# Optimization experiments

Hardware: AMD Instinct MI355X
Metric: run time of the kernel (lower is better)

The kernel has to match this reference:

```python
import jax, jax.numpy as jnp
import numpy as np

N_NODES = 50000
N_EDGES = 1600000
F_IN = 512      # 2 * embedding_dimension
HID = 512
OUT = 4
NEG_SLOPE = 0.01  # torch LeakyReLU default


def _leaky_relu(x):
    return jnp.where(x >= 0, x, NEG_SLOPE * x)


def setup_inputs() -> dict:
    key = jax.random.key(0)
    ks = jax.random.split(key, 12)
    s_in = 1.0 / np.sqrt(F_IN)
    s_h = 1.0 / np.sqrt(HID)
    return {
        "feature": jax.random.normal(ks[0], (N_NODES, F_IN), jnp.float32),
        "edge_index": jax.random.randint(ks[1], (2, N_EDGES), 0, N_NODES, jnp.int64),
        "edge_type": jax.random.randint(ks[2], (N_EDGES,), 0, 2, jnp.int64),
        # input MLP
        "W_in": jax.random.uniform(ks[3], (F_IN, HID), jnp.float32, -s_in, s_in),
        "b_in": jnp.zeros((HID,), jnp.float32),
        # sage1: lin_l (bias) on aggregated neighbors, lin_r (no bias) on self
        "W1_l": jax.random.uniform(ks[4], (HID, HID), jnp.float32, -s_h, s_h),
        "b1_l": jnp.zeros((HID,), jnp.float32),
        "W1_r": jax.random.uniform(ks[5], (HID, HID), jnp.float32, -s_h, s_h),
        # sage2
        "W2_l": jax.random.uniform(ks[6], (HID, HID), jnp.float32, -s_h, s_h),
        "b2_l": jnp.zeros((HID,), jnp.float32),
        "W2_r": jax.random.uniform(ks[7], (HID, HID), jnp.float32, -s_h, s_h),
        # output linear (hidden -> 4); note forward skips linear_relu_output1
        "W_out": jax.random.uniform(ks[8], (HID, OUT), jnp.float32, -s_h, s_h),
        "b_out": jnp.zeros((OUT,), jnp.float32),
    }


def _sage_conv(x, src, dst, W_l, b_l, W_r):
    # mean aggregation of source features onto destinations (PyG default flow)
    agg = jax.ops.segment_sum(x[src], dst, num_segments=N_NODES)  # [N, H]
    cnt = jax.ops.segment_sum(jnp.ones((src.shape[0], 1), x.dtype), dst,
                              num_segments=N_NODES)               # [N, 1]
    mean = agg / jnp.maximum(cnt, 1.0)
    return mean @ W_l + b_l + x @ W_r


def reference(feature, edge_index, edge_type,
              W_in, b_in, W1_l, b1_l, W1_r, W2_l, b2_l, W2_r, W_out, b_out):
    src, dst = edge_index[0], edge_index[1]
    x = _leaky_relu(feature.astype(jnp.float32) @ W_in + b_in)
    x = _sage_conv(x, src, dst, W1_l, b1_l, W1_r)
    # dropout is identity in eval mode
    x = _sage_conv(x, src, dst, W2_l, b2_l, W2_r)
    return x @ W_out + b_out
```

## Files before the change

### kernel.cpp

```cpp
#include <hip/hip_runtime.h>
#include <stdint.h>

#define NNODES 50000
#define NEDGES 1600000
#define HID 512
#define NEG_SLOPE 0.01f
#define NBUCK 98
#define NBLK 200
#define TILE 8000
#define NSUB 8
#define GPBLK 391
#define MROWS 50048

#define ZTOT4 263040
#define ZBLK 1028
#define TCBLK 1024
#define CABLK 12512
#define SABLK 1025
#define PREP_TC (ZBLK)
#define PREP_CA (ZBLK + TCBLK)
#define PREP_SA (ZBLK + TCBLK + CABLK)
#define PREP_FLAG (ZBLK + TCBLK + CABLK + SABLK)
#define PREP_GRID (PREP_FLAG + 1)

typedef __attribute__((ext_vector_type(8))) short bf16x8;
typedef __attribute__((ext_vector_type(8))) unsigned short u16x8;
typedef __attribute__((ext_vector_type(4))) float f32x4;

__device__ __forceinline__ unsigned short f2bf(float f) {
  unsigned int u = __builtin_bit_cast(unsigned int, f);
  u += 0x7FFFu + ((u >> 16) & 1u);
  return (unsigned short)(u >> 16);
}
__device__ __forceinline__ void gload_lds16(const void* g, void* l) {
  __builtin_amdgcn_global_load_lds(
      (const __attribute__((address_space(1))) void*)g,
      (__attribute__((address_space(3))) void*)l, 16, 0, 0);
}

__device__ __forceinline__ float wave_dot(const float* __restrict__ Arow,
                                          const float* __restrict__ B, int j) {
  int l = threadIdx.x & 63;
  float4 a0 = *reinterpret_cast<const float4*>(Arow + l * 8);
  float4 a1 = *reinterpret_cast<const float4*>(Arow + l * 8 + 4);
  const float* bb = B + (size_t)(l * 8) * 4 + j;
  float s = a0.x * bb[0] + a0.y * bb[4] + a0.z * bb[8] + a0.w * bb[12] +
            a1.x * bb[16] + a1.y * bb[20] + a1.z * bb[24] + a1.w * bb[28];
#pragma unroll
  for (int off = 1; off < 64; off <<= 1) s += __shfl_xor(s, off);
  return s;
}

__global__ __launch_bounds__(256) void prep(
    const float* __restrict__ feat, const float* __restrict__ W_in,
    const float* __restrict__ W2l, const float* __restrict__ W2r,
    const float* __restrict__ Wout, const float* __restrict__ b2l,
    const float* __restrict__ bout, const int* __restrict__ ei,
    float* __restrict__ zbase, unsigned short* __restrict__ Wt0,
    unsigned short* __restrict__ featb,
    float* __restrict__ Wlp, float* __restrict__ Wrp, float* __restrict__ bp,
    int* __restrict__ flag) {
  int blk = blockIdx.x, t = threadIdx.x;
  if (blk < PREP_TC) {
    int idx = blk * 256 + t;
    if (idx < ZTOT4) reinterpret_cast<float4*>(zbase)[idx] = {0.f, 0.f, 0.f, 0.f};
  } else if (blk < PREP_CA) {
    int i = (blk - PREP_TC) * 256 + t;
    int n = i >> 9, k = i & 511;
    Wt0[i] = f2bf(W_in[(k << 9) | n]);
  } else if (blk < PREP_SA) {
    int idx = (blk - PREP_CA) * 256 + t;
    size_t g = (size_t)idx * 8;
    int row = idx >> 6;
    u16x8 pk;
    if (row < NNODES) {
      float4 v0 = *reinterpret_cast<const float4*>(feat + g);
      float4 v1 = *reinterpret_cast<const float4*>(feat + g + 4);
      pk[0] = f2bf(v0.x); pk[1] = f2bf(v0.y); pk[2] = f2bf(v0.z); pk[3] = f2bf(v0.w);
      pk[4] = f2bf(v1.x); pk[5] = f2bf(v1.y); pk[6] = f2bf(v1.z); pk[7] = f2bf(v1.w);
    } else {
      pk = (u16x8)0;
    }
    *reinterpret_cast<u16x8*>(featb + g) = pk;
  } else if (blk < PREP_FLAG) {
    int gw = (blk - PREP_SA) * 4 + (t >> 6);
    int l = t & 63;
    if (gw < 2048) {
      float v = wave_dot(W2l + (size_t)(gw >> 2) * 512, Wout, gw & 3);
      if (l == 0) Wlp[gw] = v;
    } else if (gw < 4096) {
      int g = gw - 2048;
      float v = wave_dot(W2r + (size_t)(g >> 2) * 512, Wout, g & 3);
      if (l == 0) Wrp[g] = v;
    } else if (gw < 4100) {
      int j = gw - 4096;
      float v = wave_dot(b2l, Wout, j);
      if (l == 0) bp[j] = v + bout[j];
    }
  } else {
    if (t < 64) {
      unsigned long long m = __ballot(ei[2 * t + 1] != 0);
      if (t == 0) *flag = (m != 0ULL) ? 1 : 0;
    }
  }
}

__global__ __launch_bounds__(256) void smallB(
    const float* __restrict__ W1l, const float* __restrict__ W1r,
    const float* __restrict__ b1l,
    const float* __restrict__ Wlp, const float* __restrict__ Wrp,
    const float* __restrict__ bp,
    float* __restrict__ Pall, float* __restrict__ kb, float* __restrict__ kc) {
  int gw = blockIdx.x * 4 + (threadIdx.x >> 6);
  int l = threadIdx.x & 63;
  if (gw < 6144) {
    int k = gw / 12, jg = gw % 12;
    int g = jg >> 2, j = jg & 3;
    float v;
    if (g == 0) v = wave_dot(W1l + (size_t)k * 512, Wlp, j);
    else if (g == 1) v = wave_dot(W1r + (size_t)k * 512, Wlp, j) +
                         wave_dot(W1l + (size_t)k * 512, Wrp, j);
    else v = wave_dot(W1r + (size_t)k * 512, Wrp, j);
    if (l == 0) Pall[k * 12 + jg] = v;
  } else if (gw < 6152) {
    int i = gw - 6144, j = i & 3;
    if (i < 4) {
      float v = wave_dot(b1l, Wlp, j);
      if (l == 0) kb[j] = v;
    } else {
      float v = wave_dot(b1l, Wrp, j);
      if (l == 0) kc[j] = v + bp[j];
    }
  }
}

__global__ __launch_bounds__(256) void histk(const int* __restrict__ ei,
                                             const int* __restrict__ flag,
                                             int* __restrict__ hist) {
  __shared__ int h[NBUCK];
  int t = threadIdx.x, blk = blockIdx.x;
  for (int i = t; i < NBUCK; i += 256) h[i] = 0;
  __syncthreads();
  int f = *flag;
  int e0 = blk * TILE;
  for (int e = e0 + 2 * t; e < e0 + TILE; e += 512) {
    int d0, d1;
    if (f) {
      int2 v = *reinterpret_cast<const int2*>(&ei[(size_t)NEDGES + e]);
      d0 = v.x; d1 = v.y;
    } else {
      int4 v = *reinterpret_cast<const int4*>(&ei[2 * ((size_t)NEDGES + e)]);
      d0 = v.x; d1 = v.z;
    }
    if ((unsigned)d0 < NNODES) atomicAdd(&h[d0 >> 9], 1);
    if ((unsigned)d1 < NNODES) atomicAdd(&h[d1 >> 9], 1);
  }
  __syncthreads();
  for (int i = t; i < NBUCK; i += 256) hist[i * NBLK + blk] = h[i];
}

__global__ __launch_bounds__(512) void scanh(int* __restrict__ hist,
                                             int* __restrict__ bstart) {
  __shared__ int s[512];
  const int TOT = NBUCK * NBLK;
  const int C = 40;
  int t = threadIdx.x;
  int base = t * C;
  int sum = 0;
#pragma unroll
  for (int i = 0; i < C; i++) {
    int idx = base + i;
    sum += (idx < TOT) ? hist[idx] : 0;
  }
  s[t] = sum;
  __syncthreads();
  for (int off = 1; off < 512; off <<= 1) {
    int u = (t >= off) ? s[t - off] : 0;
    __syncthreads();
    s[t] += u;
    __syncthreads();
  }
  int run = (t > 0) ? s[t - 1] : 0;
#pragma unroll
  for (int i = 0; i < C; i++) {
    int idx = base + i;
    if (idx < TOT) {
      int v = hist[idx];
      hist[idx] = run;
      if (idx % NBLK == 0) bstart[idx / NBLK] = run;
      run += v;
    }
  }
  if (t == 511) bstart[NBUCK] = s[511];
}

__global__ __launch_bounds__(256) void binscatter(const int* __restrict__ ei,
                                                  const int* __restrict__ flag,
                                                  const int* __restrict__ hbase,
                                                  unsigned int* __restrict__ pcol) {
  __shared__ int lb[NBUCK];
  int t = threadIdx.x, blk = blockIdx.x;
  for (int i = t; i < NBUCK; i += 256) lb[i] = hbase[i * NBLK + blk];
  __syncthreads();
  int f = *flag;
  int e0 = blk * TILE;
  for (int e = e0 + 2 * t; e < e0 + TILE; e += 512) {
    int s0, s1v, d0, d1;
    if (f) {
      int2 vs = *reinterpret_cast<const int2*>(&ei[e]);
      int2 vd = *reinterpret_cast<const int2*>(&ei[(size_t)NEDGES + e]);
      s0 = vs.x; s1v = vs.y; d0 = vd.x; d1 = vd.y;
    } else {
      int4 vs = *reinterpret_cast<const int4*>(&ei[2 * (size_t)e]);
      int4 vd = *reinterpret_cast<const int4*>(&ei[2 * ((size_t)NEDGES + e)]);
      s0 = vs.x; s1v = vs.z; d0 = vd.x; d1 = vd.z;
    }
    if ((unsigned)d0 < NNODES) {
      if ((unsigned)s0 >= NNODES) s0 = 0;
      int pos = atomicAdd(&lb[d0 >> 9], 1);
      pcol[pos] = ((unsigned)(d0 & 511) << 16) | (unsigned)s0;
    }
    if ((unsigned)d1 < NNODES) {
      if ((unsigned)s1v >= NNODES) s1v = 0;
      int pos = atomicAdd(&lb[d1 >> 9], 1);
      pcol[pos] = ((unsigned)(d1 & 511) << 16) | (unsigned)s1v;
    }
  }
}

__global__ __launch_bounds__(256, 4) void gemmproj(
    const unsigned short* __restrict__ Ab, const unsigned short* __restrict__ Bt,
    const float* __restrict__ bias, const float* __restrict__ Pall,
    float* __restrict__ t0a, float* __restrict__ t0b, float* __restrict__ t0c) {
  __shared__ unsigned short As[2][128 * 32];
  __shared__ unsigned short Bs[2][128 * 32];
  __shared__ float tab[128 * 12];
  const int tid = threadIdx.x;
  const int wave = tid >> 6, lane = tid & 63;
  const int w = blockIdx.x;
  const int mt = (w & 7) + ((w >> 5) << 3);
  const int nb = (w >> 3) & 3;
  if (mt >= GPBLK) return;
  const int bm = mt * 128, bn = nb * 128;
  const int wr = wave >> 1, wc = wave & 1;
  const int r15 = lane & 15, kl = lane >> 4;
  const int srow = lane >> 2, soff = (lane & 3) * 8;
  const int c0 = wave * 2, c1 = wave * 2 + 1;
  const unsigned short* ga0 = Ab + (size_t)(bm + c0 * 16 + srow) * HID + soff;
  const unsigned short* ga1 = Ab + (size_t)(bm + c1 * 16 + srow) * HID + soff;
  const unsigned short* gb0 = Bt + (size_t)(bn + c0 * 16 + srow) * HID + soff;
  const unsigned short* gb1 = Bt + (size_t)(bn + c1 * 16 + srow) * HID + soff;

  for (int i = tid; i < 1536; i += 256) tab[i] = 0.f;

  f32x4 acc[4][4];
#pragma unroll
  for (int i = 0; i < 4; i++)
#pragma unroll
    for (int j = 0; j < 4; j++) acc[i][j] = {0.f, 0.f, 0.f, 0.f};

  gload_lds16(ga0, (void*)&As[0][c0 * 512]);
  gload_lds16(gb0, (void*)&Bs[0][c0 * 512]);
  gload_lds16(ga1, (void*)&As[0][c1 * 512]);
  gload_lds16(gb1, (void*)&Bs[0][c1 * 512]);
  __syncthreads();

  for (int kt = 0; kt < 16; ++kt) {
    const int cur = kt & 1;
    if (kt < 15) {
      const int nxt = cur ^ 1;
      const int ko = (kt + 1) * 32;
      gload_lds16(ga0 + ko, (void*)&As[nxt][c0 * 512]);
      gload_lds16(gb0 + ko, (void*)&Bs[nxt][c0 * 512]);
      gload_lds16(ga1 + ko, (void*)&As[nxt][c1 * 512]);
      gload_lds16(gb1 + ko, (void*)&Bs[nxt][c1 * 512]);
    }
    bf16x8 af[4], bfr[4];
#pragma unroll
    for (int mi = 0; mi < 4; ++mi)
      af[mi] = *reinterpret_cast<const bf16x8*>(&As[cur][(wr * 64 + mi * 16 + r15) * 32 + kl * 8]);
#pragma unroll
    for (int ni = 0; ni < 4; ++ni)
      bfr[ni] = *reinterpret_cast<const bf16x8*>(&Bs[cur][(wc * 64 + ni * 16 + r15) * 32 + kl * 8]);
#pragma unroll
    for (int ni = 0; ni < 4; ++ni)
#pragma unroll
      for (int mi = 0; mi < 4; ++mi)
        acc[ni][mi] = __builtin_amdgcn_mfma_f32_16x16x32_bf16(bfr[ni], af[mi], acc[ni][mi], 0, 0, 0);
    __syncthreads();
  }

#pragma unroll
  for (int mi = 0; mi < 4; ++mi) {
    float p12[12];
#pragma unroll
    for (int j = 0; j < 12; ++j) p12[j] = 0.f;
#pragma unroll
    for (int ni = 0; ni < 4; ++ni) {
      int nbase = bn + wc * 64 + ni * 16 + kl * 4;
      float4 bv4 = *reinterpret_cast<const float4*>(bias + nbase);
      float bb[4] = {bv4.x, bv4.y, bv4.z, bv4.w};
#pragma unroll
      for (int rg = 0; rg < 4; ++rg) {
        float v = acc[ni][mi][rg] + bb[rg];
        v = (v >= 0.f) ? v : NEG_SLOPE * v;
        const float* Pc = Pall + (size_t)(nbase + rg) * 12;
        float4 p0 = *reinterpret_cast<const float4*>(Pc);
        float4 p1 = *reinterpret_cast<const float4*>(Pc + 4);
        float4 p2 = *reinterpret_cast<const float4*>(Pc + 8);
        p12[0] += v * p0.x; p12[1] += v * p0.y; p12[2] += v * p0.z; p12[3] += v * p0.w;
        p12[4] += v * p1.x; p12[5] += v * p1.y; p12[6] += v * p1.z; p12[7] += v * p1.w;
        p12[8] += v * p2.x; p12[9] += v * p2.y; p12[10] += v * p2.z; p12[11] += v * p2.w;
      }
    }
#pragma unroll
    for (int j = 0; j < 12; ++j) {
      p12[j] += __shfl_xor(p12[j], 16);
      p12[j] += __shfl_xor(p12[j], 32);
    }
    if (kl == 0) {
      int r = wr * 64 + mi * 16 + r15;
#pragma unroll
      for (int j = 0; j < 12; ++j) atomicAdd(&tab[r * 12 + j], p12[j]);
    }
  }
  __syncthreads();
  for (int i = tid; i < 1536; i += 256) {
    int r = i / 12, j = i - r * 12;
    size_t gr = (size_t)(bm + r);
    float v = tab[i];
    if (j < 4) atomicAdd(&t0a[gr * 4 + j], v);
    else if (j < 8) atomicAdd(&t0b[gr * 4 + (j - 4)], v);
    else atomicAdd(&t0c[gr * 4 + (j - 8)], v);
  }
}

__global__ __launch_bounds__(256) void aggA(
    const unsigned int* __restrict__ pcol, const int* __restrict__ bstart,
    const float* __restrict__ t0a, float* __restrict__ accA) {
  __shared__ float tab[512 * 5];
  int t = threadIdx.x;
  int b = blockIdx.x >> 3, sb = blockIdx.x & 7;
  for (int i = t; i < 2560; i += 256) tab[i] = 0.f;
  __syncthreads();
  int st = bstart[b], en = bstart[b + 1];
  int len = en - st;
  int a0 = st + (int)(((long long)len * sb) >> 3);
  int a1 = st + (int)(((long long)len * (sb + 1)) >> 3);
  for (int e = a0 + t; e < a1; e += 256) {
    unsigned v = pcol[e];
    int i = v >> 16, src = v & 0xFFFF;
    float4 x = *reinterpret_cast<const float4*>(t0a + (size_t)src * 4);
    atomicAdd(&tab[i * 5 + 0], x.x);
    atomicAdd(&tab[i * 5 + 1], x.y);
    atomicAdd(&tab[i * 5 + 2], x.z);
    atomicAdd(&tab[i * 5 + 3], x.w);
    atomicAdd(&tab[i * 5 + 4], 1.f);
  }
  __syncthreads();
  float* o = accA + (size_t)b * 2560;
  for (int i = t; i < 2560; i += 256) {
    float v = tab[i];
    if (v != 0.f) atomicAdd(&o[i], v);
  }
}

__global__ __launch_bounds__(256) void finA(
    const float* __restrict__ accA, const float* __restrict__ t0b,
    float* __restrict__ s1, float* __restrict__ degf) {
  int n = blockIdx.x * 256 + threadIdx.x;
  if (n >= NNODES) return;
  const float* a = accA + (size_t)n * 5;
  float deg = a[4];
  float sc = (deg > 0.f) ? 1.f / deg : 0.f;
  float4 tb = *reinterpret_cast<const float4*>(t0b + (size_t)n * 4);
  float4 o = {a[0] * sc + tb.x, a[1] * sc + tb.y, a[2] * sc + tb.z, a[3] * sc + tb.w};
  *reinterpret_cast<float4*>(s1 + (size_t)n * 4) = o;
  degf[n] = deg;
}

__global__ __launch_bounds__(256) void aggB(
    const unsigned int* __restrict__ pcol, const int* __restrict__ bstart,
    const float* __restrict__ s1, float* __restrict__ accB) {
  __shared__ float tab[512 * 4];
  int t = threadIdx.x;
  int b = blockIdx.x >> 3, sb = blockIdx.x & 7;
  for (int i = t; i < 2048; i += 256) tab[i] = 0.f;
  __syncthreads();
  int st = bstart[b], en = bstart[b + 1];
  int len = en - st;
  int a0 = st + (int)(((long long)len * sb) >> 3);
  int a1 = st + (int)(((long long)len * (sb + 1)) >> 3);
  for (int e = a0 + t; e < a1; e += 256) {
    unsigned v = pcol[e];
    int i = v >> 16, src = v & 0xFFFF;
    float4 x = *reinterpret_cast<const float4*>(s1 + (size_t)src * 4);
    atomicAdd(&tab[i * 4 + 0], x.x);
    atomicAdd(&tab[i * 4 + 1], x.y);
    atomicAdd(&tab[i * 4 + 2], x.z);
    atomicAdd(&tab[i * 4 + 3], x.w);
  }
  __syncthreads();
  float* o = accB + (size_t)b * 2048;
  for (int i = t; i < 2048; i += 256) {
    float v = tab[i];
    if (v != 0.f) atomicAdd(&o[i], v);
  }
}

__global__ __launch_bounds__(256) void finB(
    const float* __restrict__ accB, const float* __restrict__ t0c,
    const float* __restrict__ degf, const float* __restrict__ kb,
    const float* __restrict__ kc, float* __restrict__ out) {
  int n = blockIdx.x * 256 + threadIdx.x;
  if (n >= NNODES) return;
  const float* a = accB + (size_t)n * 4;
  float deg = degf[n];
  float sc = (deg > 0.f) ? 1.f / deg : 0.f;
  float ind = (deg > 0.f) ? 1.f : 0.f;
  float4 c = *reinterpret_cast<const float4*>(t0c + (size_t)n * 4);
  float4 vb = *reinterpret_cast<const float4*>(kb);
  float4 vc = *reinterpret_cast<const float4*>(kc);
  float4 o = {a[0] * sc + c.x + ind * vb.x + vc.x,
              a[1] * sc + c.y + ind * vb.y + vc.y,
              a[2] * sc + c.z + ind * vb.z + vc.z,
              a[3] * sc + c.w + ind * vb.w + vc.w};
  *reinterpret_cast<float4*>(out + (size_t)n * 4) = o;
}

extern "C" void kernel_launch(void* const* d_in, const int* in_sizes, int n_in,
                              void* d_out, int out_size, void* d_ws, size_t ws_size,
                              hipStream_t stream) {
  const float* feat = (const float*)d_in[0];
  const int* ei = (const int*)d_in[1];
  const float* W_in = (const float*)d_in[3];
  const float* b_in = (const float*)d_in[4];
  const float* W1l = (const float*)d_in[5];
  const float* b1l = (const float*)d_in[6];
  const float* W1r = (const float*)d_in[7];
  const float* W2l = (const float*)d_in[8];
  const float* b2l = (const float*)d_in[9];
  const float* W2r = (const float*)d_in[10];
  const float* Wout = (const float*)d_in[11];
  const float* bout = (const float*)d_in[12];
  float* out = (float*)d_out;

  char* ws = (char*)d_ws;
  size_t off = 0;
  auto alloc = [&](size_t bytes) {
    void* p = ws + off;
    off += (bytes + 15) & ~(size_t)15;
    return p;
  };
  float* t0a  = (float*)alloc((size_t)MROWS * 4 * 4);
  float* t0b  = (float*)alloc((size_t)MROWS * 4 * 4);
  float* t0c  = (float*)alloc((size_t)MROWS * 4 * 4);
  float* accA = (float*)alloc((size_t)NBUCK * 2560 * 4);
  float* accB = (float*)alloc((size_t)NBUCK * 2048 * 4);
  float* zbase = t0a;

  int* flag   = (int*)alloc(16);
  int* hist   = (int*)alloc((size_t)NBUCK * NBLK * 4);
  int* bstart = (int*)alloc((NBUCK + 1) * 4);
  unsigned int* pcol = (unsigned int*)alloc((size_t)NEDGES * 4);
  unsigned short* featb = (unsigned short*)alloc((size_t)MROWS * HID * 2);
  unsigned short* Wt0 = (unsigned short*)alloc(512 * 512 * 2);
  float* Wlp  = (float*)alloc(2048 * 4);
  float* Wrp  = (float*)alloc(2048 * 4);
  float* bp   = (float*)alloc(16);
  float* Pall = (float*)alloc(512 * 12 * 4);
  float* kb   = (float*)alloc(16);
  float* kc   = (float*)alloc(16);
  float* s1   = (float*)alloc((size_t)MROWS * 4 * 4);
  float* degf = (float*)alloc((size_t)NNODES * 4);
  (void)ws_size;

  prep<<<PREP_GRID, 256, 0, stream>>>(feat, W_in, W2l, W2r, Wout, b2l, bout, ei,
                                      zbase, Wt0, featb, Wlp, Wrp, bp, flag);
  smallB<<<1538, 256, 0, stream>>>(W1l, W1r, b1l, Wlp, Wrp, bp, Pall, kb, kc);

  histk<<<NBLK, 256, 0, stream>>>(ei, flag, hist);
  scanh<<<1, 512, 0, stream>>>(hist, bstart);
  binscatter<<<NBLK, 256, 0, stream>>>(ei, flag, hist, pcol);

  gemmproj<<<1568, 256, 0, stream>>>(featb, Wt0, b_in, Pall, t0a, t0b, t0c);
  aggA<<<NBUCK * NSUB, 256, 0, stream>>>(pcol, bstart, t0a, accA);
  finA<<<(NNODES + 255) / 256, 256, 0, stream>>>(accA, t0b, s1, degf);
  aggB<<<NBUCK * NSUB, 256, 0, stream>>>(pcol, bstart, s1, accB);
  finB<<<(NNODES + 255) / 256, 256, 0, stream>>>(accB, t0c, degf, kb, kc, out);
}
```

Before: 289.1 us.

## Stage binscatter output in LDS and widen GEMM K-tile to 64

Binscatter now sorts each tile's edges by bucket in shared memory and then writes them to global memory in contiguous runs, instead of issuing scattered global stores. This is meant to improve write coalescing. The edge-index dtype flag is now computed locally in histk and binscatter rather than by a prep block, which removes a global dependency. The GEMM drops the double-buffered 32-wide K pipeline for a single-buffered 64-wide K tile, giving half as many barriers per pass but losing overlap between loads and MFMA work.

```diff
diff --git a/kernel.cpp b/kernel.cpp
--- a/kernel.cpp
+++ b/kernel.cpp
@@ -20,8 +20,7 @@
 #define PREP_TC (ZBLK)
 #define PREP_CA (ZBLK + TCBLK)
 #define PREP_SA (ZBLK + TCBLK + CABLK)
-#define PREP_FLAG (ZBLK + TCBLK + CABLK + SABLK)
-#define PREP_GRID (PREP_FLAG + 1)
+#define PREP_GRID (PREP_SA + SABLK)
 
 typedef __attribute__((ext_vector_type(8))) short bf16x8;
 typedef __attribute__((ext_vector_type(8))) unsigned short u16x8;
@@ -55,11 +54,10 @@
     const float* __restrict__ feat, const float* __restrict__ W_in,
     const float* __restrict__ W2l, const float* __restrict__ W2r,
     const float* __restrict__ Wout, const float* __restrict__ b2l,
-    const float* __restrict__ bout, const int* __restrict__ ei,
+    const float* __restrict__ bout,
     float* __restrict__ zbase, unsigned short* __restrict__ Wt0,
     unsigned short* __restrict__ featb,
-    float* __restrict__ Wlp, float* __restrict__ Wrp, float* __restrict__ bp,
-    int* __restrict__ flag) {
+    float* __restrict__ Wlp, float* __restrict__ Wrp, float* __restrict__ bp) {
   int blk = blockIdx.x, t = threadIdx.x;
   if (blk < PREP_TC) {
     int idx = blk * 256 + t;
@@ -82,7 +80,7 @@
       pk = (u16x8)0;
     }
     *reinterpret_cast<u16x8*>(featb + g) = pk;
-  } else if (blk < PREP_FLAG) {
+  } else {
     int gw = (blk - PREP_SA) * 4 + (t >> 6);
     int l = t & 63;
     if (gw < 2048) {
@@ -96,11 +94,6 @@
       int j = gw - 4096;
       float v = wave_dot(b2l, Wout, j);
       if (l == 0) bp[j] = v + bout[j];
-    }
-  } else {
-    if (t < 64) {
-      unsigned long long m = __ballot(ei[2 * t + 1] != 0);
-      if (t == 0) *flag = (m != 0ULL) ? 1 : 0;
     }
   }
 }
@@ -135,13 +128,17 @@
 }
 
 __global__ __launch_bounds__(256) void histk(const int* __restrict__ ei,
-                                             const int* __restrict__ flag,
                                              int* __restrict__ hist) {
   __shared__ int h[NBUCK];
+  __shared__ int flg;
   int t = threadIdx.x, blk = blockIdx.x;
   for (int i = t; i < NBUCK; i += 256) h[i] = 0;
-  __syncthreads();
-  int f = *flag;
+  if (t < 64) {
+    unsigned long long m = __ballot(ei[2 * t + 1] != 0);
+    if (t == 0) flg = (m != 0ULL) ? 1 : 0;
+  }
+  __syncthreads();
+  int f = flg;
   int e0 = blk * TILE;
   for (int e = e0 + 2 * t; e < e0 + TILE; e += 512) {
     int d0, d1;
@@ -195,15 +192,46 @@
 }
 
 __global__ __launch_bounds__(256) void binscatter(const int* __restrict__ ei,
-                                                  const int* __restrict__ flag,
                                                   const int* __restrict__ hbase,
                                                   unsigned int* __restrict__ pcol) {
-  __shared__ int lb[NBUCK];
+  __shared__ unsigned int vals[TILE];
+  __shared__ unsigned char bid[TILE];
+  __shared__ int lcnt[NBUCK];
+  __shared__ int lbase[NBUCK];
+  __shared__ int delta[NBUCK];
+  __shared__ int flg;
   int t = threadIdx.x, blk = blockIdx.x;
-  for (int i = t; i < NBUCK; i += 256) lb[i] = hbase[i * NBLK + blk];
-  __syncthreads();
-  int f = *flag;
+  for (int i = t; i < NBUCK; i += 256) lcnt[i] = 0;
+  if (t < 64) {
+    unsigned long long m = __ballot(ei[2 * t + 1] != 0);
+    if (t == 0) flg = (m != 0ULL) ? 1 : 0;
+  }
+  __syncthreads();
+  int f = flg;
   int e0 = blk * TILE;
+  for (int e = e0 + 2 * t; e < e0 + TILE; e += 512) {
+    int d0, d1;
+    if (f) {
+      int2 vd = *reinterpret_cast<const int2*>(&ei[(size_t)NEDGES + e]);
+      d0 = vd.x; d1 = vd.y;
+    } else {
+      int4 vd = *reinterpret_cast<const int4*>(&ei[2 * ((size_t)NEDGES + e)]);
+      d0 = vd.x; d1 = vd.z;
+    }
+    if ((unsigned)d0 < NNODES) atomicAdd(&lcnt[d0 >> 9], 1);
+    if ((unsigned)d1 < NNODES) atomicAdd(&lcnt[d1 >> 9], 1);
+  }
+  __syncthreads();
+  if (t == 0) {
+    int run = 0;
+    for (int b = 0; b < NBUCK; b++) { lbase[b] = run; run += lcnt[b]; }
+  }
+  __syncthreads();
+  for (int b = t; b < NBUCK; b += 256) {
+    delta[b] = hbase[b * NBLK + blk] - lbase[b];
+    lcnt[b] = 0;
+  }
+  __syncthreads();
   for (int e = e0 + 2 * t; e < e0 + TILE; e += 512) {
     int s0, s1v, d0, d1;
     if (f) {
@@ -217,14 +245,23 @@
     }
     if ((unsigned)d0 < NNODES) {
       if ((unsigned)s0 >= NNODES) s0 = 0;
-      int pos = atomicAdd(&lb[d0 >> 9], 1);
-      pcol[pos] = ((unsigned)(d0 & 511) << 16) | (unsigned)s0;
+      int b = d0 >> 9;
+      int p = lbase[b] + atomicAdd(&lcnt[b], 1);
+      vals[p] = ((unsigned)(d0 & 511) << 16) | (unsigned)s0;
+      bid[p] = (unsigned char)b;
     }
     if ((unsigned)d1 < NNODES) {
       if ((unsigned)s1v >= NNODES) s1v = 0;
-      int pos = atomicAdd(&lb[d1 >> 9], 1);
-      pcol[pos] = ((unsigned)(d1 & 511) << 16) | (unsigned)s1v;
-    }
+      int b = d1 >> 9;
+      int p = lbase[b] + atomicAdd(&lcnt[b], 1);
+      vals[p] = ((unsigned)(d1 & 511) << 16) | (unsigned)s1v;
+      bid[p] = (unsigned char)b;
+    }
+  }
+  __syncthreads();
+  int total = lbase[NBUCK - 1] + lcnt[NBUCK - 1];
+  for (int p = t; p < total; p += 256) {
+    pcol[delta[bid[p]] + p] = vals[p];
   }
 }
 
@@ -232,8 +269,8 @@
     const unsigned short* __restrict__ Ab, const unsigned short* __restrict__ Bt,
     const float* __restrict__ bias, const float* __restrict__ Pall,
     float* __restrict__ t0a, float* __restrict__ t0b, float* __restrict__ t0c) {
-  __shared__ unsigned short As[2][128 * 32];
-  __shared__ unsigned short Bs[2][128 * 32];
+  __shared__ unsigned short As[128 * 64];
+  __shared__ unsigned short Bs[128 * 64];
   __shared__ float tab[128 * 12];
   const int tid = threadIdx.x;
   const int wave = tid >> 6, lane = tid & 63;
@@ -244,12 +281,8 @@
   const int bm = mt * 128, bn = nb * 128;
   const int wr = wave >> 1, wc = wave & 1;
   const int r15 = lane & 15, kl = lane >> 4;
-  const int srow = lane >> 2, soff = (lane & 3) * 8;
-  const int c0 = wave * 2, c1 = wave * 2 + 1;
-  const unsigned short* ga0 = Ab + (size_t)(bm + c0 * 16 + srow) * HID + soff;
-  const unsigned short* ga1 = Ab + (size_t)(bm + c1 * 16 + srow) * HID + soff;
-  const unsigned short* gb0 = Bt + (size_t)(bn + c0 * 16 + srow) * HID + soff;
-  const unsigned short* gb1 = Bt + (size_t)(bn + c1 * 16 + srow) * HID + soff;
+  const int srow = lane >> 3;
+  const int soff = (lane & 7) * 8;
 
   for (int i = tid; i < 1536; i += 256) tab[i] = 0.f;
 
@@ -259,34 +292,30 @@
 #pragma unroll
     for (int j = 0; j < 4; j++) acc[i][j] = {0.f, 0.f, 0.f, 0.f};
 
-  gload_lds16(ga0, (void*)&As[0][c0 * 512]);
-  gload_lds16(gb0, (void*)&Bs[0][c0 * 512]);
-  gload_lds16(ga1, (void*)&As[0][c1 * 512]);
-  gload_lds16(gb1, (void*)&Bs[0][c1 * 512]);
-  __syncthreads();
-
-  for (int kt = 0; kt < 16; ++kt) {
-    const int cur = kt & 1;
-    if (kt < 15) {
-      const int nxt = cur ^ 1;
-      const int ko = (kt + 1) * 32;
-      gload_lds16(ga0 + ko, (void*)&As[nxt][c0 * 512]);
-      gload_lds16(gb0 + ko, (void*)&Bs[nxt][c0 * 512]);
-      gload_lds16(ga1 + ko, (void*)&As[nxt][c1 * 512]);
-      gload_lds16(gb1 + ko, (void*)&Bs[nxt][c1 * 512]);
-    }
-    bf16x8 af[4], bfr[4];
-#pragma unroll
-    for (int mi = 0; mi < 4; ++mi)
-      af[mi] = *reinterpret_cast<const bf16x8*>(&As[cur][(wr * 64 + mi * 16 + r15) * 32 + kl * 8]);
-#pragma unroll
-    for (int ni = 0; ni < 4; ++ni)
-      bfr[ni] = *reinterpret_cast<const bf16x8*>(&Bs[cur][(wc * 64 + ni * 16 + r15) * 32 + kl * 8]);
-#pragma unroll
-    for (int ni = 0; ni < 4; ++ni)
+  for (int kt = 0; kt < 8; ++kt) {
+#pragma unroll
+    for (int q = 0; q < 4; ++q) {
+      int c = wave * 4 + q;
+      int row = c * 8 + srow;
+      gload_lds16(Ab + (size_t)(bm + row) * HID + kt * 64 + soff, (void*)&As[c * 512]);
+      gload_lds16(Bt + (size_t)(bn + row) * HID + kt * 64 + soff, (void*)&Bs[c * 512]);
+    }
+    __syncthreads();
+#pragma unroll
+    for (int k2 = 0; k2 < 2; ++k2) {
+      bf16x8 af[4], bfr[4];
 #pragma unroll
       for (int mi = 0; mi < 4; ++mi)
-        acc[ni][mi] = __builtin_amdgcn_mfma_f32_16x16x32_bf16(bfr[ni], af[mi], acc[ni][mi], 0, 0, 0);
+        af[mi] = *reinterpret_cast<const bf16x8*>(&As[(wr * 64 + mi * 16 + r15) * 64 + k2 * 32 + kl * 8]);
+#pragma unroll
+      for (int ni = 0; ni < 4; ++ni)
+        bfr[ni] = *reinterpret_cast<const bf16x8*>(&Bs[(wc * 64 + ni * 16 + r15) * 64 + k2 * 32 + kl * 8]);
+#pragma unroll
+      for (int ni = 0; ni < 4; ++ni)
+#pragma unroll
+        for (int mi = 0; mi < 4; ++mi)
+          acc[ni][mi] = __builtin_amdgcn_mfma_f32_16x16x32_bf16(bfr[ni], af[mi], acc[ni][mi], 0, 0, 0);
+    }
     __syncthreads();
   }
 
@@ -459,7 +488,6 @@
   float* accB = (float*)alloc((size_t)NBUCK * 2048 * 4);
   float* zbase = t0a;
 
-  int* flag   = (int*)alloc(16);
   int* hist   = (int*)alloc((size_t)NBUCK * NBLK * 4);
   int* bstart = (int*)alloc((NBUCK + 1) * 4);
   unsigned int* pcol = (unsigned int*)alloc((size_t)NEDGES * 4);
@@ -475,13 +503,13 @@
   float* degf = (float*)alloc((size_t)NNODES * 4);
   (void)ws_size;
 
-  prep<<<PREP_GRID, 256, 0, stream>>>(feat, W_in, W2l, W2r, Wout, b2l, bout, ei,
-                                      zbase, Wt0, featb, Wlp, Wrp, bp, flag);
+  prep<<<PREP_GRID, 256, 0, stream>>>(feat, W_in, W2l, W2r, Wout, b2l, bout,
+                                      zbase, Wt0, featb, Wlp, Wrp, bp);
   smallB<<<1538, 256, 0, stream>>>(W1l, W1r, b1l, Wlp, Wrp, bp, Pall, kb, kc);
 
-  histk<<<NBLK, 256, 0, stream>>>(ei, flag, hist);
+  histk<<<NBLK, 256, 0, stream>>>(ei, hist);
   scanh<<<1, 512, 0, stream>>>(hist, bstart);
-  binscatter<<<NBLK, 256, 0, stream>>>(ei, flag, hist, pcol);
+  binscatter<<<NBLK, 256, 0, stream>>>(ei, hist, pcol);
 
   gemmproj<<<1568, 256, 0, stream>>>(featb, Wt0, b_in, Pall, t0a, t0b, t0c);
   aggA<<<NBUCK * NSUB, 256, 0, stream>>>(pcol, bstart, t0a, accA);
```

New measurement: 306.1 us. 5.9% more time.
